# Performance work log

Hardware: AMD Instinct MI355X
Metric: run time of the kernel (lower is better)

## Reference

```python
import jax, jax.numpy as jnp
import numpy as np

B, T, D = 8, 4096, 64

def setup_inputs() -> dict:
    key = jax.random.key(0)
    k1, k2 = jax.random.split(key)
    inputs = jax.random.normal(k1, (B, T, D), dtype=jnp.float32)
    # keras 'random_normal' initializer: stddev 0.05
    W = jax.random.normal(k2, (D, D), dtype=jnp.float32) * 0.05
    return {"inputs": inputs, "W": W}

def reference(inputs, W):
    # q = inputs @ W               : [B,T,D]
    # a = q @ inputs^T             : [B,T,T] (no scaling, bias b unused in original)
    # out = softmax(a, -1) @ inputs: [B,T,D]
    q = jnp.einsum('btd,de->bte', inputs, W)
    scores = jnp.einsum('btd,bsd->bts', q, inputs)
    attn = jax.nn.softmax(scores, axis=-1)
    return jnp.einsum('bts,bsd->btd', attn, inputs)
```

## Files before the change

kernel.cpp:

```cpp
#include <hip/hip_runtime.h>

typedef _Float16 f16;
typedef _Float16 f16x8 __attribute__((ext_vector_type(8)));
typedef __bf16 bf16x8 __attribute__((ext_vector_type(8)));
typedef float floatx4 __attribute__((ext_vector_type(4)));
typedef unsigned short u16;

#define B_N   8
#define T_SEQ 4096
#define DIM   64
#define QT    64
#define NIT   32
#define XSTR  72
#define LOG2E 1.44269504f
#define FRAG  512

#if __has_builtin(__builtin_amdgcn_exp2f)
#define EXP2(x) __builtin_amdgcn_exp2f(x)
#else
#define EXP2(x) exp2f(x)
#endif

typedef __attribute__((address_space(1))) const void gvoid;
typedef __attribute__((address_space(3))) void svoid;

__launch_bounds__(256, 4)
__global__ void prep_kernel(const float* __restrict__ X, const float* __restrict__ W,
                            u16* __restrict__ Kswz, u16* __restrict__ Qswz,
                            u16* __restrict__ Vswz) {
  __shared__ __attribute__((aligned(16))) u16 Xs[32 * XSTR];
  __shared__ __attribute__((aligned(16))) u16 Wt[DIM * XSTR];
  __shared__ __attribute__((aligned(16))) u16 Qs[2][16 * XSTR];
  const int tid = threadIdx.x;
  const int lane = tid & 63, w = tid >> 6, qd = lane >> 4, ln = lane & 15;
  const int b = blockIdx.y;
  const int tau = blockIdx.x;
  const long xbase = ((long)b * T_SEQ + tau * 32) * DIM;

  {
    const int r = tid >> 3, c0 = (tid & 7) * 8;
    float v[8];
    *(float4*)&v[0] = *(const float4*)(X + xbase + (long)r * DIM + c0);
    *(float4*)&v[4] = *(const float4*)(X + xbase + (long)r * DIM + c0 + 4);
    u16 h[8];
#pragma unroll
    for (int j = 0; j < 8; j++) h[j] = __builtin_bit_cast(u16, (f16)v[j]);
    *(uint4*)&Xs[r * XSTR + c0] = *(uint4*)&h[0];
    const int r2 = tid >> 2, c2 = (tid & 3) * 16;
    float wv[16];
#pragma unroll
    for (int i = 0; i < 4; i++)
      *(float4*)&wv[i * 4] = *(const float4*)(W + r2 * DIM + c2 + i * 4);
#pragma unroll
    for (int j = 0; j < 16; j++) Wt[(c2 + j) * XSTR + r2] = __builtin_bit_cast(u16, (f16)wv[j]);
  }
  __syncthreads();

  if (w == 0) {
#pragma unroll
    for (int ct = 0; ct < 2; ct++) {
      const int krow = (ln >> 2) * 8 + ct * 4 + (ln & 3);
      const long F = ((long)b * 128 + tau) * 2 + ct;
#pragma unroll
      for (int ks = 0; ks < 2; ks++) {
        f16x8 kv = *(const f16x8*)&Xs[krow * XSTR + ks * 32 + qd * 8];
        *(f16x8*)(Kswz + (F * 2 + ks) * FRAG + lane * 8) = kv;
      }
    }
    {
      const long Cb = (long)b * 4 + 0;
      bf16x8 vv;
#pragma unroll
      for (int j = 0; j < 8; j++) {
        f16 hv = __builtin_bit_cast(f16, Xs[(qd * 8 + j) * XSTR + 0 * 16 + ln]);
        vv[j] = (__bf16)(float)hv;
      }
      *(bf16x8*)(Vswz + (Cb * (T_SEQ / 32) + tau) * FRAG + lane * 8) = vv;
    }
  } else if (w == 1) {
#pragma unroll
    for (int db = 1; db < 4; db++) {
      const long Cb = (long)b * 4 + db;
      bf16x8 vv;
#pragma unroll
      for (int j = 0; j < 8; j++) {
        f16 hv = __builtin_bit_cast(f16, Xs[(qd * 8 + j) * XSTR + db * 16 + ln]);
        vv[j] = (__bf16)(float)hv;
      }
      *(bf16x8*)(Vswz + (Cb * (T_SEQ / 32) + tau) * FRAG + lane * 8) = vv;
    }
  } else {
    const int h2 = w - 2;
    const int rq = h2 * 16;
    floatx4 acc[4];
#pragma unroll
    for (int ct = 0; ct < 4; ct++) acc[ct] = (floatx4)0.0f;
#pragma unroll
    for (int ks = 0; ks < 2; ks++) {
      f16x8 aX = *(const f16x8*)&Xs[(rq + ln) * XSTR + ks * 32 + qd * 8];
#pragma unroll
      for (int ct = 0; ct < 4; ct++) {
        f16x8 bW = *(const f16x8*)&Wt[(ct * 16 + ln) * XSTR + ks * 32 + qd * 8];
        acc[ct] = __builtin_amdgcn_mfma_f32_16x16x32_f16(aX, bW, acc[ct], 0, 0, 0);
      }
    }
#pragma unroll
    for (int ct = 0; ct < 4; ct++)
#pragma unroll
      for (int r = 0; r < 4; r++)
        Qs[h2][(qd * 4 + r) * XSTR + ct * 16 + ln] =
            __builtin_bit_cast(u16, (f16)(acc[ct][r] * LOG2E));
    const long R = (long)b * (T_SEQ / 16) + tau * 2 + h2;
#pragma unroll
    for (int ks = 0; ks < 2; ks++) {
      f16x8 qv = *(const f16x8*)&Qs[h2][ln * XSTR + ks * 32 + qd * 8];
      *(f16x8*)(Qswz + (R * 2 + ks) * FRAG + lane * 8) = qv;
    }
  }
}

__launch_bounds__(512, 4)
__global__ void attn_kernel(const u16* __restrict__ Kswz, const u16* __restrict__ Qswz,
                            const u16* __restrict__ Vswz, float* __restrict__ out) {
  __shared__ __attribute__((aligned(16))) char sbuf[2][32768];
  __shared__ float lpart[8][32];
  float* Opart = (float*)&sbuf[0][0];

  const int tid = threadIdx.x;
  const int lane = tid & 63;
  const int w = tid >> 6;
  const int qd = lane >> 4;
  const int ln = lane & 15;
  const int wg = w >> 2;
  const int wk = w & 3;
  const int bid = blockIdx.x;
  const int b = bid & 7;
  const int q0 = (bid >> 3) * QT;
  const long bbase = (long)b * T_SEQ * DIM;

  f16x8 aQ[2][2];
#pragma unroll
  for (int rb = 0; rb < 2; rb++)
#pragma unroll
    for (int ks = 0; ks < 2; ks++)
      aQ[rb][ks] = *(const f16x8*)(Qswz +
          (((long)b * (T_SEQ / 16) + (q0 >> 4) + wg * 2 + rb) * 2 + ks) * FRAG + lane * 8);

  const char* gKw = (const char*)Kswz + (long)b * 524288 + (long)w * 4096 + lane * 16;
  const char* gVw = (const char*)Vswz + (long)b * 524288 + (long)(w - 4) * 1024 + lane * 16;

#define STAGE(bufv, t)                                                                  \
  do {                                                                                  \
    if (w < 4) {                                                                        \
      const char* g = gKw + (long)(t) * 16384;                                          \
      char* l = &sbuf[bufv][w * 4096];                                                  \
      _Pragma("unroll") for (int i = 0; i < 4; i++)                                     \
          __builtin_amdgcn_global_load_lds((gvoid*)(g + i * 1024), (svoid*)(l + i * 1024), \
                                           16, 0, 0);                                   \
    } else {                                                                            \
      const char* g = gVw + (long)(t) * 4096;                                           \
      char* l = &sbuf[bufv][16384 + (w - 4) * 4096];                                    \
      _Pragma("unroll") for (int i = 0; i < 4; i++)                                     \
          __builtin_amdgcn_global_load_lds((gvoid*)(g + i * 131072), (svoid*)(l + i * 1024), \
                                           16, 0, 0);                                   \
    }                                                                                   \
  } while (0)

  floatx4 O[2][4];
  float lacc[2] = {0.f, 0.f};
#pragma unroll
  for (int rb = 0; rb < 2; rb++)
#pragma unroll
    for (int db = 0; db < 4; db++) O[rb][db] = (floatx4)0.0f;

  STAGE(0, 0);
  __syncthreads();

  int buf = 0;
#pragma unroll 1
  for (int t = 0; t < NIT; t++) {
    if (t + 1 < NIT) STAGE(buf ^ 1, t + 1);

    const char* Kb = &sbuf[buf][wk * 4096];
    const char* Vb = &sbuf[buf][16384 + wk * 4096];
    f16x8 bK[2][2];
#pragma unroll
    for (int ct = 0; ct < 2; ct++)
#pragma unroll
      for (int ks = 0; ks < 2; ks++)
        bK[ct][ks] = *(const f16x8*)(Kb + (ct * 2 + ks) * 1024 + lane * 16);
    bf16x8 bV[4];
#pragma unroll
    for (int db = 0; db < 4; db++)
      bV[db] = *(const bf16x8*)(Vb + db * 1024 + lane * 16);

    floatx4 St[2][2];
#pragma unroll
    for (int ct = 0; ct < 2; ct++)
#pragma unroll
      for (int rb = 0; rb < 2; rb++) St[ct][rb] = (floatx4)0.0f;
    __builtin_amdgcn_s_setprio(1);
#pragma unroll
    for (int ks = 0; ks < 2; ks++)
#pragma unroll
      for (int ct = 0; ct < 2; ct++)
#pragma unroll
        for (int rb = 0; rb < 2; rb++)
          St[ct][rb] = __builtin_amdgcn_mfma_f32_16x16x32_f16(bK[ct][ks], aQ[rb][ks], St[ct][rb], 0, 0, 0);
    __builtin_amdgcn_s_setprio(0);

    bf16x8 pk[2];
#pragma unroll
    for (int rb = 0; rb < 2; rb++) {
      float ps = 0.f;
#pragma unroll
      for (int ct = 0; ct < 2; ct++)
#pragma unroll
        for (int r = 0; r < 4; r++) {
          float p = EXP2(St[ct][rb][r]);
          ps += p;
          pk[rb][ct * 4 + r] = (__bf16)p;
        }
      lacc[rb] += ps;
    }

    __builtin_amdgcn_s_setprio(1);
#pragma unroll
    for (int rb = 0; rb < 2; rb++)
#pragma unroll
      for (int db = 0; db < 4; db++)
        O[rb][db] = __builtin_amdgcn_mfma_f32_16x16x32_bf16(pk[rb], bV[db], O[rb][db], 0, 0, 0);
    __builtin_amdgcn_s_setprio(0);

    __syncthreads();
    buf ^= 1;
  }

#pragma unroll
  for (int rb = 0; rb < 2; rb++) {
    float v = lacc[rb];
    v += __shfl_xor(v, 16, 64);
    v += __shfl_xor(v, 32, 64);
    if (qd == 0) lpart[w][rb * 16 + ln] = v;
  }

#pragma unroll
  for (int rb = 0; rb < 2; rb++) {
    __syncthreads();
#pragma unroll
    for (int db = 0; db < 4; db++)
#pragma unroll
      for (int r = 0; r < 4; r++)
        Opart[(w * 16 + qd * 4 + r) * 68 + db * 16 + ln] = O[rb][db][r];
    __syncthreads();
    const int wg2 = tid >> 8;
    const int q2 = (tid >> 4) & 15;
    const int d0 = (tid & 15) * 4;
    float4 s = *(const float4*)&Opart[((wg2 * 4 + 0) * 16 + q2) * 68 + d0];
    const float4 s1 = *(const float4*)&Opart[((wg2 * 4 + 1) * 16 + q2) * 68 + d0];
    const float4 s2 = *(const float4*)&Opart[((wg2 * 4 + 2) * 16 + q2) * 68 + d0];
    const float4 s3 = *(const float4*)&Opart[((wg2 * 4 + 3) * 16 + q2) * 68 + d0];
    float l = lpart[wg2 * 4 + 0][rb * 16 + q2] + lpart[wg2 * 4 + 1][rb * 16 + q2] +
              lpart[wg2 * 4 + 2][rb * 16 + q2] + lpart[wg2 * 4 + 3][rb * 16 + q2];
    const float inv = 1.0f / l;
    float4 o;
    o.x = (s.x + s1.x + s2.x + s3.x) * inv;
    o.y = (s.y + s1.y + s2.y + s3.y) * inv;
    o.z = (s.z + s1.z + s2.z + s3.z) * inv;
    o.w = (s.w + s1.w + s2.w + s3.w) * inv;
    *(float4*)(out + bbase + (long)(q0 + wg2 * 32 + rb * 16 + q2) * DIM + d0) = o;
  }
#undef STAGE
}

extern "C" void kernel_launch(void* const* d_in, const int* in_sizes, int n_in,
                              void* d_out, int out_size, void* d_ws, size_t ws_size,
                              hipStream_t stream) {
  const float* X = (const float*)d_in[0];
  const float* W = (const float*)d_in[1];
  float* out = (float*)d_out;
  const size_t SZ = (size_t)B_N * T_SEQ * DIM * 2;
  u16* Kswz = (u16*)d_ws;
  u16* Qswz = (u16*)((char*)d_ws + SZ);
  u16* Vswz = (u16*)((char*)d_ws + 2 * SZ);
  prep_kernel<<<dim3(T_SEQ / 32, B_N), 256, 0, stream>>>(X, W, Kswz, Qswz, Vswz);
  attn_kernel<<<dim3(B_N * (T_SEQ / QT)), 512, 0, stream>>>(Kswz, Qswz, Vswz, out);
}
```

Before: 106.1 us.

## Software-pipeline PV MFMA of previous tile with QK MFMA and exp of current tile

Restructures the attention loop so each iteration issues the P·V MFMAs for the previous key tile before computing the S=QK scores and exponentials for the current tile. P and V fragments are double-buffered in registers (A/B sets), and the loop is unrolled by two to swap them. The aim is to let the exp/convert ALU work overlap with independent MFMA work instead of waiting on a serial dependency. It raises register pressure, adds a prologue and epilogue, and could reduce occupancy.

```diff
diff --git a/kernel.cpp b/kernel.cpp
--- a/kernel.cpp
+++ b/kernel.cpp
@@ -173,68 +173,66 @@
 #pragma unroll
     for (int db = 0; db < 4; db++) O[rb][db] = (floatx4)0.0f;
 
+  bf16x8 pkA[2], pkB[2];
+  bf16x8 bVA[4], bVB[4];
+
+#define STEP(t, bufv, IN, OUT, DO_PV, DO_STAGE)                                         \
+  do {                                                                                  \
+    if (DO_STAGE) STAGE((bufv) ^ 1, (t) + 1);                                           \
+    const char* Kb_ = &sbuf[bufv][wk * 4096];                                           \
+    const char* Vb_ = &sbuf[bufv][16384 + wk * 4096];                                   \
+    f16x8 bK_[2][2];                                                                    \
+    _Pragma("unroll") for (int ct = 0; ct < 2; ct++)                                    \
+      _Pragma("unroll") for (int ks = 0; ks < 2; ks++)                                  \
+        bK_[ct][ks] = *(const f16x8*)(Kb_ + (ct * 2 + ks) * 1024 + lane * 16);          \
+    _Pragma("unroll") for (int db = 0; db < 4; db++)                                    \
+      bV##OUT[db] = *(const bf16x8*)(Vb_ + db * 1024 + lane * 16);                      \
+    __builtin_amdgcn_s_setprio(1);                                                      \
+    if (DO_PV) {                                                                        \
+      _Pragma("unroll") for (int rb = 0; rb < 2; rb++)                                  \
+        _Pragma("unroll") for (int db = 0; db < 4; db++)                                \
+          O[rb][db] = __builtin_amdgcn_mfma_f32_16x16x32_bf16(pk##IN[rb], bV##IN[db],   \
+                                                              O[rb][db], 0, 0, 0);      \
+    }                                                                                   \
+    floatx4 St_[2][2];                                                                  \
+    _Pragma("unroll") for (int ct = 0; ct < 2; ct++)                                    \
+      _Pragma("unroll") for (int rb = 0; rb < 2; rb++) St_[ct][rb] = (floatx4)0.0f;     \
+    _Pragma("unroll") for (int ks = 0; ks < 2; ks++)                                    \
+      _Pragma("unroll") for (int ct = 0; ct < 2; ct++)                                  \
+        _Pragma("unroll") for (int rb = 0; rb < 2; rb++)                                \
+          St_[ct][rb] = __builtin_amdgcn_mfma_f32_16x16x32_f16(bK_[ct][ks], aQ[rb][ks], \
+                                                               St_[ct][rb], 0, 0, 0);   \
+    __builtin_amdgcn_s_setprio(0);                                                      \
+    _Pragma("unroll") for (int rb = 0; rb < 2; rb++) {                                  \
+      float ps = 0.f;                                                                   \
+      _Pragma("unroll") for (int ct = 0; ct < 2; ct++)                                  \
+        _Pragma("unroll") for (int r = 0; r < 4; r++) {                                 \
+          float p = EXP2(St_[ct][rb][r]);                                               \
+          ps += p;                                                                      \
+          pk##OUT[rb][ct * 4 + r] = (__bf16)p;                                          \
+        }                                                                               \
+      lacc[rb] += ps;                                                                   \
+    }                                                                                   \
+    __syncthreads();                                                                    \
+  } while (0)
+
   STAGE(0, 0);
   __syncthreads();
 
-  int buf = 0;
+  STEP(0, 0, A, A, 0, 1);
 #pragma unroll 1
-  for (int t = 0; t < NIT; t++) {
-    if (t + 1 < NIT) STAGE(buf ^ 1, t + 1);
-
-    const char* Kb = &sbuf[buf][wk * 4096];
-    const char* Vb = &sbuf[buf][16384 + wk * 4096];
-    f16x8 bK[2][2];
-#pragma unroll
-    for (int ct = 0; ct < 2; ct++)
-#pragma unroll
-      for (int ks = 0; ks < 2; ks++)
-        bK[ct][ks] = *(const f16x8*)(Kb + (ct * 2 + ks) * 1024 + lane * 16);
-    bf16x8 bV[4];
+  for (int t = 1; t < 31; t += 2) {
+    STEP(t, 1, A, B, 1, 1);
+    STEP(t + 1, 0, B, A, 1, 1);
+  }
+  STEP(31, 1, A, B, 1, 0);
+  __builtin_amdgcn_s_setprio(1);
+#pragma unroll
+  for (int rb = 0; rb < 2; rb++)
 #pragma unroll
     for (int db = 0; db < 4; db++)
-      bV[db] = *(const bf16x8*)(Vb + db * 1024 + lane * 16);
-
-    floatx4 St[2][2];
-#pragma unroll
-    for (int ct = 0; ct < 2; ct++)
-#pragma unroll
-      for (int rb = 0; rb < 2; rb++) St[ct][rb] = (floatx4)0.0f;
-    __builtin_amdgcn_s_setprio(1);
-#pragma unroll
-    for (int ks = 0; ks < 2; ks++)
-#pragma unroll
-      for (int ct = 0; ct < 2; ct++)
-#pragma unroll
-        for (int rb = 0; rb < 2; rb++)
-          St[ct][rb] = __builtin_amdgcn_mfma_f32_16x16x32_f16(bK[ct][ks], aQ[rb][ks], St[ct][rb], 0, 0, 0);
-    __builtin_amdgcn_s_setprio(0);
-
-    bf16x8 pk[2];
-#pragma unroll
-    for (int rb = 0; rb < 2; rb++) {
-      float ps = 0.f;
-#pragma unroll
-      for (int ct = 0; ct < 2; ct++)
-#pragma unroll
-        for (int r = 0; r < 4; r++) {
-          float p = EXP2(St[ct][rb][r]);
-          ps += p;
-          pk[rb][ct * 4 + r] = (__bf16)p;
-        }
-      lacc[rb] += ps;
-    }
-
-    __builtin_amdgcn_s_setprio(1);
-#pragma unroll
-    for (int rb = 0; rb < 2; rb++)
-#pragma unroll
-      for (int db = 0; db < 4; db++)
-        O[rb][db] = __builtin_amdgcn_mfma_f32_16x16x32_bf16(pk[rb], bV[db], O[rb][db], 0, 0, 0);
-    __builtin_amdgcn_s_setprio(0);
-
-    __syncthreads();
-    buf ^= 1;
-  }
+      O[rb][db] = __builtin_amdgcn_mfma_f32_16x16x32_bf16(pkB[rb], bVB[db], O[rb][db], 0, 0, 0);
+  __builtin_amdgcn_s_setprio(0);
 
 #pragma unroll
   for (int rb = 0; rb < 2; rb++) {
@@ -270,6 +268,7 @@
     o.w = (s.w + s1.w + s2.w + s3.w) * inv;
     *(float4*)(out + bbase + (long)(q0 + wg2 * 32 + rb * 16 + q2) * DIM + d0) = o;
   }
+#undef STEP
 #undef STAGE
 }
 
```

New measurement: 141.0 us. 32.9% more time.
